# Optimization experiments

Measured on AMD Instinct MI355X. Metric: run time of the kernel, lower is better.

Reference implementation:

```python
import math
import jax, jax.numpy as jnp
import numpy as np

NUM_HEADS = 16
D_MODEL = 1024
WINDOW = 512


def alibi_slopes(num_heads):
    # 1 / ((2**8)**((i+1)/num_heads))  for i in range(num_heads)
    x = (2.0 ** 8) ** (1.0 / num_heads)
    return jnp.asarray([1.0 / x ** (i + 1) for i in range(num_heads)], dtype=jnp.float32)


def setup_inputs() -> dict:
    key = jax.random.key(0)
    k1, k2 = jax.random.split(key)
    x = jax.random.normal(k1, (1, 4096, D_MODEL), dtype=jnp.float32)
    # scale weight like a trained init so softmax isn't saturated
    w_kqv = jax.random.normal(k2, (D_MODEL, 3 * D_MODEL), dtype=jnp.float32) * 0.02
    return {"x": x, "w_kqv": w_kqv}


def reference(x, w_kqv):
    B, S, D = x.shape
    H = NUM_HEADS
    hd = D // H
    scale = math.sqrt(D)  # module scales by sqrt(d_model), not sqrt(head_dim)

    kqv = x @ w_kqv                       # [B, S, 3D]
    k, q, v = jnp.split(kqv, 3, axis=-1)  # chunk order: key, query, value
    k = k.reshape(B, S, H, hd).transpose(0, 2, 1, 3)  # [B, H, S, hd]
    q = q.reshape(B, S, H, hd).transpose(0, 2, 1, 3)
    v = v.reshape(B, S, H, hd).transpose(0, 2, 1, 3)

    # ALiBi bias: m_h * (j - i)
    pos = jnp.arange(S)
    rel = pos[None, :] - pos[:, None]                  # [S, S] = x - y
    bias = alibi_slopes(H)[:, None, None] * rel.astype(jnp.float32)  # [H, S, S]

    score = jnp.einsum("bhqd,bhkd->bhqk", q, k) / scale + bias[None]

    # causal sliding-window mask: allow 0 <= i - j <= WINDOW
    dist = pos[:, None] - pos[None, :]                 # i - j
    mask = (dist >= 0) & (dist <= WINDOW)              # [S, S]
    score = jnp.where(mask[None, None], score, -jnp.inf)

    attn = jax.nn.softmax(score, axis=-1)
    out = jnp.einsum("bhqk,bhkd->bhqd", attn, v)       # [B, H, S, hd]
    out = out.transpose(0, 2, 1, 3).reshape(B, S, D)
    return out
```

## Files before the change

### kernel.cpp

```cpp
#include <hip/hip_runtime.h>
#include <hip/hip_bf16.h>

#define SEQ   4096
#define DM    1024
#define NH    16
#define HD    64
#define N3    3072
#define WIN   512

#define LOG2E 1.4426950408889634f

typedef __attribute__((ext_vector_type(8))) short short8;
typedef __attribute__((ext_vector_type(4))) short short4v;
typedef __attribute__((ext_vector_type(4))) float float4v;

__device__ __forceinline__ float bf16_bits_to_float(unsigned short u) {
  return __uint_as_float(((unsigned int)u) << 16);
}

typedef __attribute__((address_space(3))) void lds_void_t;
typedef __attribute__((address_space(1))) const void gbl_void_t;
__device__ __forceinline__ void async_copy16(void* lds_dst, const void* g_src) {
  __builtin_amdgcn_global_load_lds((gbl_void_t*)g_src, (lds_void_t*)lds_dst,
                                   16, 0, 0);
}

template <int NT>
__device__ __forceinline__ int detect_fp32(const unsigned short* __restrict__ probe,
                                           float* red) {
  const int t = threadIdx.x;
  float mx = 0.0f;
#pragma unroll
  for (int p = 0; p < 8; ++p) {
    float v = bf16_bits_to_float(probe[(t * 8 + p) * 2]);
    if (v != v) v = 1e38f;
    mx = fmaxf(mx, fabsf(v));
  }
  red[t] = mx;
  __syncthreads();
  for (int s = NT / 2; s > 0; s >>= 1) {
    if (t < s) red[t] = fmaxf(red[t], red[t + s]);
    __syncthreads();
  }
  const int fl = red[0] > 100.0f ? 1 : 0;
  __syncthreads();
  return fl;
}

__global__ __launch_bounds__(256) void prep(
    const void* __restrict__ x, const void* __restrict__ w,
    __hip_bfloat16* __restrict__ xb, __hip_bfloat16* __restrict__ wt) {
  __shared__ __hip_bfloat16 tile[64][66];
  __shared__ float red[256];
  const int t = threadIdx.x;
  if (blockIdx.x < 2048) {
    const int fl = detect_fp32<256>((const unsigned short*)x, red);
    const int i0 = (blockIdx.x * 256 + t) * 8;
    if (fl) {
      const float* xf = (const float*)x + i0;
      float4 f0 = *(const float4*)(xf);
      float4 f1 = *(const float4*)(xf + 4);
      __hip_bfloat16 tmp[8];
      tmp[0] = __float2bfloat16(f0.x); tmp[1] = __float2bfloat16(f0.y);
      tmp[2] = __float2bfloat16(f0.z); tmp[3] = __float2bfloat16(f0.w);
      tmp[4] = __float2bfloat16(f1.x); tmp[5] = __float2bfloat16(f1.y);
      tmp[6] = __float2bfloat16(f1.z); tmp[7] = __float2bfloat16(f1.w);
      *(uint4*)&xb[i0] = *(const uint4*)tmp;
    } else {
      *(uint4*)&xb[i0] = *(const uint4*)((const __hip_bfloat16*)x + i0);
    }
  } else {
    const int bid = blockIdx.x - 2048;
    const int fl = detect_fp32<256>((const unsigned short*)w, red);
    const int n0 = (bid % 48) * 64;
    const int k0 = (bid / 48) * 64;
    const int tx = t & 63, ty0 = t >> 6;
    if (fl) {
      const float* wf = (const float*)w;
#pragma unroll
      for (int p = 0; p < 16; ++p) {
        int row = ty0 + p * 4;
        tile[row][tx] = __float2bfloat16(wf[(k0 + row) * N3 + n0 + tx]);
      }
    } else {
      const __hip_bfloat16* wb = (const __hip_bfloat16*)w;
#pragma unroll
      for (int p = 0; p < 16; ++p) {
        int row = ty0 + p * 4;
        tile[row][tx] = wb[(k0 + row) * N3 + n0 + tx];
      }
    }
    __syncthreads();
#pragma unroll
    for (int r = 0; r < 2; ++r) {
      int oe = r * 2048 + t * 8;
      int nr = oe >> 6, kc = oe & 63;
      __hip_bfloat16 v[8];
#pragma unroll
      for (int e = 0; e < 8; ++e) v[e] = tile[kc + e][nr];
      *(uint4*)&wt[(n0 + nr) * DM + k0 + kc] = *(const uint4*)v;
    }
  }
}

__global__ __launch_bounds__(256) void gemm_kqv(
    const __hip_bfloat16* __restrict__ A,
    const __hip_bfloat16* __restrict__ BT,
    __hip_bfloat16* __restrict__ C) {
  __shared__ __align__(16) __hip_bfloat16 As[2][128 * 32];
  __shared__ __align__(16) __hip_bfloat16 Bs[2][128 * 32];
  const int m0 = blockIdx.y * 128;
  const int n0 = blockIdx.x * 128;
  const int t = threadIdx.x;
  const int wave = t >> 6, lane = t & 63;
  const int wm = wave >> 1, wn = wave & 1;
  const int l15 = lane & 15, quad = lane >> 4;

  const int srow0 = wave * 16 + (lane >> 2);
  const int scol  = (lane & 3) * 8;
  const int sbyte = wave * 1024 + lane * 16;

  float4v acc[4][4] = {};

  for (int k0 = 0; k0 < DM; k0 += 64) {
    __syncthreads();
#pragma unroll
    for (int half = 0; half < 2; ++half) {
      const int kk = k0 + half * 32;
#pragma unroll
      for (int r = 0; r < 2; ++r) {
        const int row = srow0 + r * 64;
        async_copy16((char*)As[half] + r * 4096 + sbyte,
                     &A[(m0 + row) * DM + kk + scol]);
        async_copy16((char*)Bs[half] + r * 4096 + sbyte,
                     &BT[(n0 + row) * DM + kk + scol]);
      }
    }
    __syncthreads();

#pragma unroll
    for (int half = 0; half < 2; ++half) {
      short8 a[4], b[4];
#pragma unroll
      for (int mi = 0; mi < 4; ++mi)
        a[mi] = *(const short8*)(&As[half][(wm * 64 + mi * 16 + l15) * 32 + quad * 8]);
#pragma unroll
      for (int ni = 0; ni < 4; ++ni)
        b[ni] = *(const short8*)(&Bs[half][(wn * 64 + ni * 16 + l15) * 32 + quad * 8]);
#pragma unroll
      for (int mi = 0; mi < 4; ++mi)
#pragma unroll
        for (int ni = 0; ni < 4; ++ni)
          acc[mi][ni] = __builtin_amdgcn_mfma_f32_16x16x32_bf16(
              a[mi], b[ni], acc[mi][ni], 0, 0, 0);
    }
  }

#pragma unroll
  for (int mi = 0; mi < 4; ++mi)
#pragma unroll
    for (int ni = 0; ni < 4; ++ni)
#pragma unroll
      for (int r = 0; r < 4; ++r) {
        int row = m0 + wm * 64 + mi * 16 + quad * 4 + r;
        int col = n0 + wn * 64 + ni * 16 + l15;
        C[row * N3 + col] = __float2bfloat16(acc[mi][ni][r]);
      }
}

__global__ __launch_bounds__(256, 4) void attn(
    const __hip_bfloat16* __restrict__ kqv,
    const unsigned short* __restrict__ xprobe,
    void* __restrict__ out) {
  __shared__ __align__(16) __hip_bfloat16 Ks[64 * 72];
  __shared__ __align__(16) __hip_bfloat16 Vt[80 * 68];
  __shared__ __align__(16) __hip_bfloat16 Ps[64 * 72];
  __shared__ float red[256];

  const int fl = detect_fp32<256>(xprobe, red);
  const int h  = blockIdx.y;
  const int bx = blockIdx.x;
  const int i0 = 64 * ((bx & 7) * 8 + (bx >> 3));
  const int t    = threadIdx.x;
  const int wave = t >> 6, lane = t & 63;
  const int l15 = lane & 15, quad = lane >> 4;
  const float slope2  = exp2f(-0.5f * (float)(h + 1)) * LOG2E;
  const float nslope2 = -slope2;
  const float qscale  = LOG2E / 32.0f;

  for (int idx = t; idx < 16 * 68; idx += 256) {
    int rr = idx / 68, cc = idx - rr * 68;
    ((unsigned short*)Vt)[(64 + rr) * 68 + cc] = (rr == 0) ? 0x3F80 : 0;
  }

  short8 aq[2];
#pragma unroll
  for (int ks2 = 0; ks2 < 2; ++ks2)
    aq[ks2] = *(const short8*)&kqv[(i0 + wave * 16 + l15) * N3 + DM + h * HD +
                                   ks2 * 32 + quad * 8];

  float4v o[5] = {};

  const int jlo  = max(0, i0 - WIN);
  const int nblk = (i0 + 64 - jlo) >> 6;

  const int krow0 = t >> 3, krow1 = (t >> 3) + 32, kd0 = (t & 7) * 8;
  const int vr0 = (t >> 3) * 2, vd0 = (t & 7) * 8;
  uint4 kregA, kregB, vregA, vregB;
  kregA = *(const uint4*)&kqv[(jlo + krow0) * N3 + h * HD + kd0];
  kregB = *(const uint4*)&kqv[(jlo + krow1) * N3 + h * HD + kd0];
  vregA = *(const uint4*)&kqv[(jlo + vr0) * N3 + 2 * DM + h * HD + vd0];
  vregB = *(const uint4*)&kqv[(jlo + vr0 + 1) * N3 + 2 * DM + h * HD + vd0];

  for (int b = 0; b < nblk; ++b) {
    const int j0 = jlo + b * 64;
    __syncthreads();
    *(uint4*)&Ks[krow0 * 72 + kd0] = kregA;
    *(uint4*)&Ks[krow1 * 72 + kd0] = kregB;
    {
      const unsigned short* pa = (const unsigned short*)&vregA;
      const unsigned short* pb = (const unsigned short*)&vregB;
#pragma unroll
      for (int e = 0; e < 8; ++e) {
        unsigned int pack = (unsigned int)pa[e] | ((unsigned int)pb[e] << 16);
        *(unsigned int*)&Vt[(vd0 + e) * 68 + vr0] = pack;
      }
    }
    if (b + 1 < nblk) {
      const int jn = j0 + 64;
      kregA = *(const uint4*)&kqv[(jn + krow0) * N3 + h * HD + kd0];
      kregB = *(const uint4*)&kqv[(jn + krow1) * N3 + h * HD + kd0];
      vregA = *(const uint4*)&kqv[(jn + vr0) * N3 + 2 * DM + h * HD + vd0];
      vregB = *(const uint4*)&kqv[(jn + vr0 + 1) * N3 + 2 * DM + h * HD + vd0];
    }
    __syncthreads();

    float4v sacc[4] = {};
#pragma unroll
    for (int ks2 = 0; ks2 < 2; ++ks2)
#pragma unroll
      for (int nt = 0; nt < 4; ++nt) {
        short8 bk = *(const short8*)&Ks[(nt * 16 + l15) * 72 + ks2 * 32 + quad * 8];
        sacc[nt] = __builtin_amdgcn_mfma_f32_16x16x32_bf16(aq[ks2], bk, sacc[nt], 0, 0, 0);
      }

    const int dbase = (i0 + wave * 16 + quad * 4) - (j0 + l15);
    const float s16 = nslope2 * -16.0f;
#pragma unroll
    for (int r = 0; r < 4; ++r) {
      float bias = nslope2 * (float)(dbase + r);
      int rel = dbase + r;
#pragma unroll
      for (int nt = 0; nt < 4; ++nt) {
        float x = fmaf(sacc[nt][r], qscale, bias);
        x = ((unsigned)rel <= (unsigned)WIN) ? x : -200.0f;
        Ps[(wave * 16 + quad * 4 + r) * 72 + nt * 16 + l15] =
            __float2bfloat16(exp2f(x));
        bias += s16;
        rel -= 16;
      }
    }

#pragma unroll
    for (int ks = 0; ks < 64; ks += 32) {
      short8 ap = *(const short8*)&Ps[(wave * 16 + l15) * 72 + ks + quad * 8];
#pragma unroll
      for (int dt = 0; dt < 5; ++dt) {
        const __hip_bfloat16* vp = &Vt[(dt * 16 + l15) * 68 + ks + quad * 8];
        short4v v0 = *(const short4v*)vp;
        short4v v1 = *(const short4v*)(vp + 4);
        short8 bv = __builtin_shufflevector(v0, v1, 0, 1, 2, 3, 4, 5, 6, 7);
        o[dt] = __builtin_amdgcn_mfma_f32_16x16x32_bf16(ap, bv, o[dt], 0, 0, 0);
      }
    }
  }

#pragma unroll
  for (int r = 0; r < 4; ++r) {
    const float l = __shfl(o[4][r], quad * 16, 64);
    const float inv_l = 1.0f / l;
    const int row = i0 + wave * 16 + quad * 4 + r;
#pragma unroll
    for (int dt = 0; dt < 4; ++dt) {
      const int idx = row * DM + h * HD + dt * 16 + l15;
      const float v = o[dt][r] * inv_l;
      if (fl) ((float*)out)[idx] = v;
      else    ((__hip_bfloat16*)out)[idx] = __float2bfloat16(v);
    }
  }
}

extern "C" void kernel_launch(void* const* d_in, const int* in_sizes, int n_in,
                              void* d_out, int out_size, void* d_ws, size_t ws_size,
                              hipStream_t stream) {
  char* ws = (char*)d_ws;
  __hip_bfloat16* wt  = (__hip_bfloat16*)(ws + 4096);
  __hip_bfloat16* kqv = (__hip_bfloat16*)(ws + 4096 + 6291456);
  __hip_bfloat16* xb  = (__hip_bfloat16*)d_out;

  hipLaunchKernelGGL(prep, dim3(2048 + 768), dim3(256), 0, stream,
                     d_in[0], d_in[1], xb, wt);
  hipLaunchKernelGGL(gemm_kqv, dim3(24, 32), dim3(256), 0, stream, xb, wt, kqv);
  hipLaunchKernelGGL(attn, dim3(64, 16), dim3(256), 0, stream,
                     kqv, (const unsigned short*)d_in[0], d_out);
}
```

Measured before the change: 148.9 us.

## Double-buffer K/V tiles in LDS and use a wave-level fp32 probe

The attention loop now keeps two LDS buffers for K and transposed V and a two-deep register prefetch. The next tile is written into the idle buffer after the current tile's compute, which cuts the loop to one block barrier per tile instead of two. The fp32 input detection switches from a block-wide LDS reduction with barriers to a per-wave __any vote, and the ones row used for the softmax denominator moves to its own LDS array. Launch bounds drop from 4 to 3 blocks per SM because LDS use and register pressure both grow, which may lower occupancy.

```diff
diff --git a/kernel.cpp b/kernel.cpp
--- a/kernel.cpp
+++ b/kernel.cpp
@@ -45,6 +45,19 @@
   const int fl = red[0] > 100.0f ? 1 : 0;
   __syncthreads();
   return fl;
+}
+
+__device__ __forceinline__ int detect_fp32_wave(
+    const unsigned short* __restrict__ probe) {
+  const int lane = threadIdx.x & 63;
+  float mx = 0.0f;
+#pragma unroll
+  for (int p = 0; p < 8; ++p) {
+    float v = bf16_bits_to_float(probe[(lane * 8 + p) * 2]);
+    if (v != v) v = 1e38f;
+    mx = fmaxf(mx, fabsf(v));
+  }
+  return __any(mx > 100.0f) ? 1 : 0;
 }
 
 __global__ __launch_bounds__(256) void prep(
@@ -168,16 +181,21 @@
       }
 }
 
-__global__ __launch_bounds__(256, 4) void attn(
+#define KS_STRIDE 72
+#define VT_STRIDE 68
+#define KS_SZ (64 * KS_STRIDE)
+#define VT_SZ (64 * VT_STRIDE)
+
+__global__ __launch_bounds__(256, 3) void attn(
     const __hip_bfloat16* __restrict__ kqv,
     const unsigned short* __restrict__ xprobe,
     void* __restrict__ out) {
-  __shared__ __align__(16) __hip_bfloat16 Ks[64 * 72];
-  __shared__ __align__(16) __hip_bfloat16 Vt[80 * 68];
-  __shared__ __align__(16) __hip_bfloat16 Ps[64 * 72];
-  __shared__ float red[256];
-
-  const int fl = detect_fp32<256>(xprobe, red);
+  __shared__ __align__(16) __hip_bfloat16 Ks[2 * KS_SZ];
+  __shared__ __align__(16) __hip_bfloat16 Vt[2 * VT_SZ];
+  __shared__ __align__(16) __hip_bfloat16 Ones[16 * VT_STRIDE];
+  __shared__ __align__(16) __hip_bfloat16 Ps[64 * KS_STRIDE];
+
+  const int fl = detect_fp32_wave(xprobe);
   const int h  = blockIdx.y;
   const int bx = blockIdx.x;
   const int i0 = 64 * ((bx & 7) * 8 + (bx >> 3));
@@ -188,9 +206,9 @@
   const float nslope2 = -slope2;
   const float qscale  = LOG2E / 32.0f;
 
-  for (int idx = t; idx < 16 * 68; idx += 256) {
-    int rr = idx / 68, cc = idx - rr * 68;
-    ((unsigned short*)Vt)[(64 + rr) * 68 + cc] = (rr == 0) ? 0x3F80 : 0;
+  for (int idx = t; idx < 16 * VT_STRIDE; idx += 256) {
+    int rr = idx / VT_STRIDE;
+    ((unsigned short*)Ones)[idx] = (rr == 0) ? 0x3F80 : 0;
   }
 
   short8 aq[2];
@@ -206,74 +224,112 @@
 
   const int krow0 = t >> 3, krow1 = (t >> 3) + 32, kd0 = (t & 7) * 8;
   const int vr0 = (t >> 3) * 2, vd0 = (t & 7) * 8;
-  uint4 kregA, kregB, vregA, vregB;
-  kregA = *(const uint4*)&kqv[(jlo + krow0) * N3 + h * HD + kd0];
-  kregB = *(const uint4*)&kqv[(jlo + krow1) * N3 + h * HD + kd0];
-  vregA = *(const uint4*)&kqv[(jlo + vr0) * N3 + 2 * DM + h * HD + vd0];
-  vregB = *(const uint4*)&kqv[(jlo + vr0 + 1) * N3 + 2 * DM + h * HD + vd0];
-
-  for (int b = 0; b < nblk; ++b) {
-    const int j0 = jlo + b * 64;
-    __syncthreads();
-    *(uint4*)&Ks[krow0 * 72 + kd0] = kregA;
-    *(uint4*)&Ks[krow1 * 72 + kd0] = kregB;
-    {
-      const unsigned short* pa = (const unsigned short*)&vregA;
-      const unsigned short* pb = (const unsigned short*)&vregB;
-#pragma unroll
-      for (int e = 0; e < 8; ++e) {
-        unsigned int pack = (unsigned int)pa[e] | ((unsigned int)pb[e] << 16);
-        *(unsigned int*)&Vt[(vd0 + e) * 68 + vr0] = pack;
-      }
-    }
-    if (b + 1 < nblk) {
-      const int jn = j0 + 64;
-      kregA = *(const uint4*)&kqv[(jn + krow0) * N3 + h * HD + kd0];
-      kregB = *(const uint4*)&kqv[(jn + krow1) * N3 + h * HD + kd0];
-      vregA = *(const uint4*)&kqv[(jn + vr0) * N3 + 2 * DM + h * HD + vd0];
-      vregB = *(const uint4*)&kqv[(jn + vr0 + 1) * N3 + 2 * DM + h * HD + vd0];
-    }
-    __syncthreads();
-
-    float4v sacc[4] = {};
-#pragma unroll
-    for (int ks2 = 0; ks2 < 2; ++ks2)
-#pragma unroll
-      for (int nt = 0; nt < 4; ++nt) {
-        short8 bk = *(const short8*)&Ks[(nt * 16 + l15) * 72 + ks2 * 32 + quad * 8];
-        sacc[nt] = __builtin_amdgcn_mfma_f32_16x16x32_bf16(aq[ks2], bk, sacc[nt], 0, 0, 0);
-      }
-
-    const int dbase = (i0 + wave * 16 + quad * 4) - (j0 + l15);
-    const float s16 = nslope2 * -16.0f;
-#pragma unroll
-    for (int r = 0; r < 4; ++r) {
-      float bias = nslope2 * (float)(dbase + r);
-      int rel = dbase + r;
-#pragma unroll
-      for (int nt = 0; nt < 4; ++nt) {
-        float x = fmaf(sacc[nt][r], qscale, bias);
-        x = ((unsigned)rel <= (unsigned)WIN) ? x : -200.0f;
-        Ps[(wave * 16 + quad * 4 + r) * 72 + nt * 16 + l15] =
-            __float2bfloat16(exp2f(x));
-        bias += s16;
-        rel -= 16;
-      }
-    }
-
-#pragma unroll
-    for (int ks = 0; ks < 64; ks += 32) {
-      short8 ap = *(const short8*)&Ps[(wave * 16 + l15) * 72 + ks + quad * 8];
-#pragma unroll
-      for (int dt = 0; dt < 5; ++dt) {
-        const __hip_bfloat16* vp = &Vt[(dt * 16 + l15) * 68 + ks + quad * 8];
-        short4v v0 = *(const short4v*)vp;
-        short4v v1 = *(const short4v*)(vp + 4);
-        short8 bv = __builtin_shufflevector(v0, v1, 0, 1, 2, 3, 4, 5, 6, 7);
-        o[dt] = __builtin_amdgcn_mfma_f32_16x16x32_bf16(ap, bv, o[dt], 0, 0, 0);
-      }
-    }
-  }
+
+  uint4 kreg[2][2], vreg[2][2];
+  kreg[0][0] = *(const uint4*)&kqv[(jlo + krow0) * N3 + h * HD + kd0];
+  kreg[0][1] = *(const uint4*)&kqv[(jlo + krow1) * N3 + h * HD + kd0];
+  vreg[0][0] = *(const uint4*)&kqv[(jlo + vr0) * N3 + 2 * DM + h * HD + vd0];
+  vreg[0][1] = *(const uint4*)&kqv[(jlo + vr0 + 1) * N3 + 2 * DM + h * HD + vd0];
+  {
+    const int j1 = jlo + ((nblk > 1) ? 64 : 0);
+    kreg[1][0] = *(const uint4*)&kqv[(j1 + krow0) * N3 + h * HD + kd0];
+    kreg[1][1] = *(const uint4*)&kqv[(j1 + krow1) * N3 + h * HD + kd0];
+    vreg[1][0] = *(const uint4*)&kqv[(j1 + vr0) * N3 + 2 * DM + h * HD + vd0];
+    vreg[1][1] = *(const uint4*)&kqv[(j1 + vr0 + 1) * N3 + 2 * DM + h * HD + vd0];
+  }
+  *(uint4*)&Ks[krow0 * KS_STRIDE + kd0] = kreg[0][0];
+  *(uint4*)&Ks[krow1 * KS_STRIDE + kd0] = kreg[0][1];
+  {
+    const unsigned short* pa = (const unsigned short*)&vreg[0][0];
+    const unsigned short* pb = (const unsigned short*)&vreg[0][1];
+#pragma unroll
+    for (int e = 0; e < 8; ++e) {
+      unsigned int pack = (unsigned int)pa[e] | ((unsigned int)pb[e] << 16);
+      *(unsigned int*)&Vt[(vd0 + e) * VT_STRIDE + vr0] = pack;
+    }
+  }
+  __syncthreads();
+
+#define ATTN_STEP(B, CUR)                                                      \
+  {                                                                            \
+       \
+    if ((B) + 2 < nblk) {                                                      \
+      const int jn = jlo + ((B) + 2) * 64;                                     \
+      kreg[CUR][0] = *(const uint4*)&kqv[(jn + krow0) * N3 + h * HD + kd0];    \
+      kreg[CUR][1] = *(const uint4*)&kqv[(jn + krow1) * N3 + h * HD + kd0];    \
+      vreg[CUR][0] = *(const uint4*)&kqv[(jn + vr0) * N3 + 2 * DM + h * HD + vd0];      \
+      vreg[CUR][1] = *(const uint4*)&kqv[(jn + vr0 + 1) * N3 + 2 * DM + h * HD + vd0];  \
+    }                                                                          \
+    const int j0 = jlo + (B) * 64;                                             \
+    const __hip_bfloat16* KsC = Ks + (CUR) * KS_SZ;                            \
+    const __hip_bfloat16* VtC = Vt + (CUR) * VT_SZ;                            \
+                                                                \
+    float4v sacc[4] = {};                                                      \
+    _Pragma("unroll")                                                          \
+    for (int ks2 = 0; ks2 < 2; ++ks2) {                                        \
+      _Pragma("unroll")                                                        \
+      for (int nt = 0; nt < 4; ++nt) {                                         \
+        short8 bk = *(const short8*)&KsC[(nt * 16 + l15) * KS_STRIDE +         \
+                                         ks2 * 32 + quad * 8];                 \
+        sacc[nt] = __builtin_amdgcn_mfma_f32_16x16x32_bf16(aq[ks2], bk,        \
+                                                           sacc[nt], 0, 0, 0); \
+      }                                                                        \
+    }                                                                          \
+                                                        \
+    const int dbase = (i0 + wave * 16 + quad * 4) - (j0 + l15);                \
+    const float s16 = nslope2 * -16.0f;                                        \
+    _Pragma("unroll")                                                          \
+    for (int r = 0; r < 4; ++r) {                                              \
+      float bias = nslope2 * (float)(dbase + r);                               \
+      int rel = dbase + r;                                                     \
+      _Pragma("unroll")                                                        \
+      for (int nt = 0; nt < 4; ++nt) {                                         \
+        float x = fmaf(sacc[nt][r], qscale, bias);                             \
+        x = ((unsigned)rel <= (unsigned)WIN) ? x : -200.0f;                    \
+        Ps[(wave * 16 + quad * 4 + r) * KS_STRIDE + nt * 16 + l15] =           \
+            __float2bfloat16(exp2f(x));                                        \
+        bias += s16;                                                           \
+        rel -= 16;                                                             \
+      }                                                                        \
+    }                                                                          \
+                                                      \
+    _Pragma("unroll")                                                          \
+    for (int ks = 0; ks < 64; ks += 32) {                                      \
+      short8 ap = *(const short8*)&Ps[(wave * 16 + l15) * KS_STRIDE + ks +     \
+                                      quad * 8];                               \
+      _Pragma("unroll")                                                        \
+      for (int dt = 0; dt < 5; ++dt) {                                         \
+        const __hip_bfloat16* vp =                                             \
+            (dt < 4) ? &VtC[(dt * 16 + l15) * VT_STRIDE + ks + quad * 8]       \
+                     : &Ones[l15 * VT_STRIDE + ks + quad * 8];                 \
+        short4v v0 = *(const short4v*)vp;                                      \
+        short4v v1 = *(const short4v*)(vp + 4);                                \
+        short8 bv = __builtin_shufflevector(v0, v1, 0, 1, 2, 3, 4, 5, 6, 7);   \
+        o[dt] = __builtin_amdgcn_mfma_f32_16x16x32_bf16(ap, bv, o[dt], 0, 0, 0); \
+      }                                                                        \
+    }                                                                          \
+    \
+    if ((B) + 1 < nblk) {                                                      \
+      __hip_bfloat16* KsN = Ks + (1 - (CUR)) * KS_SZ;                          \
+      __hip_bfloat16* VtN = Vt + (1 - (CUR)) * VT_SZ;                          \
+      *(uint4*)&KsN[krow0 * KS_STRIDE + kd0] = kreg[1 - (CUR)][0];             \
+      *(uint4*)&KsN[krow1 * KS_STRIDE + kd0] = kreg[1 - (CUR)][1];             \
+      const unsigned short* pa = (const unsigned short*)&vreg[1 - (CUR)][0];   \
+      const unsigned short* pb = (const unsigned short*)&vreg[1 - (CUR)][1];   \
+      _Pragma("unroll")                                                        \
+      for (int e = 0; e < 8; ++e) {                                            \
+        unsigned int pack = (unsigned int)pa[e] | ((unsigned int)pb[e] << 16); \
+        *(unsigned int*)&VtN[(vd0 + e) * VT_STRIDE + vr0] = pack;              \
+      }                                                                        \
+    }                                                                          \
+    __syncthreads();                                                           \
+  }
+
+  for (int b = 0; b < nblk; b += 2) {
+    ATTN_STEP(b, 0);
+    if (b + 1 < nblk) ATTN_STEP(b + 1, 1);
+  }
+#undef ATTN_STEP
 
 #pragma unroll
   for (int r = 0; r < 4; ++r) {
```

Result: slower. 161.8 us (+8.7%).
